# Kernel optimization log

Hardware: AMD Instinct MI355X
Metric: run time of the kernel (lower is better)

Reference implementation:

```python
import jax, jax.numpy as jnp
import numpy as np
from jax import lax

T = 50
THETA = 1.0 - 0.0001  # max_1 - 0.0001, max_1 = T_win/T = 1.0


def conv_t(x, w, b, pad_h):
    # x: [N, C, H, W, T]; slayer conv3d has time-kernel 1 -> conv2d per timestep.
    n, c, h, wd, t = x.shape
    xb = jnp.moveaxis(x, -1, 1).reshape(n * t, c, h, wd)
    y = lax.conv_general_dilated(xb, w, (1, 1), [(pad_h, pad_h), (0, 0)])
    y = y + b[None, :, None, None]
    o, h2, w2 = y.shape[1], y.shape[2], y.shape[3]
    return jnp.moveaxis(y.reshape(n, t, o, h2, w2), 1, -1)


def if_spikes(a):
    # catCuda.getSpikes on an input stacked T times: IF neuron with constant
    # drive a per step, soft reset (v -= theta on spike). a: [N,C,H,W].
    def step(v, _):
        v = v + a
        s = (v >= THETA).astype(a.dtype)
        return v - s * THETA, s
    _, sp = lax.scan(step, jnp.zeros_like(a), None, length=T)
    return jnp.moveaxis(sp, 0, -1)  # [N,C,H,W,T]


def setup_inputs() -> dict:
    key = jax.random.key(0)
    ks = jax.random.split(key, 6)
    def w(k, shape, scale):
        return jax.random.normal(k, shape, jnp.float32) * scale
    x = jax.random.uniform(ks[0], (256, 1, 180, 1, T), jnp.float32)
    return {
        'x': x,
        'w1': w(ks[1], (16, 1, 3, 1), 0.3), 'b1': jnp.zeros(16, jnp.float32),
        'w2': w(ks[2], (32, 16, 9, 1), 0.1), 'b2': jnp.zeros(32, jnp.float32),
        'w3': w(ks[3], (32, 32, 7, 1), 0.1), 'b3': jnp.zeros(32, jnp.float32),
        'wf': w(ks[4], (4, 32, 83, 1), 0.05), 'bf': jnp.zeros(4, jnp.float32),
    }


def reference(x, w1, b1, w2, b2, w3, b3, wf, bf):
    y = conv_t(x, w1, b1, 1)                        # [N,16,180,1,T]
    y = if_spikes(jnp.sum(y, axis=4) / T)           # rate -> spikes
    y = conv_t(y, w2, b2, 1)                        # [N,32,174,1,T]
    y = if_spikes(jnp.sum(y, axis=4) / T)
    y = 1.1 * (y[:, :, 0::2] + y[:, :, 1::2])       # slayer sum-pool (2,1), weight 1.1
    y = if_spikes(jnp.sum(y, axis=4) / T)           # [N,32,87,1,T]
    y = conv_t(y, w3, b3, 1)                        # [N,32,83,1,T]
    y = if_spikes(jnp.sum(y, axis=4) / T)
    out = jnp.einsum('nchwt,ochw->not', y, wf) + bf[None, :, None]  # dense over full spatial
    return jnp.sum(out, axis=-1) / T                # sum_spikes / T -> [N,4]
```

## Files before the change

### kernel.cpp

```cpp
#include <hip/hip_runtime.h>


#define T_STEPS 50
#define THETA   0.9999f

__device__ __forceinline__ float spike_rate(float a) {
    constexpr float INV = 50.0f / 0.9999f;
    float t = a * INV;
    float c = fminf(fmaxf(floorf(t), 0.0f), 50.0f);
    bool risky = (t > 0.5f) && (fabsf(t - rintf(t)) < 5e-4f);
    if (__ballot(risky)) {
        float v = 0.f, cnt = 0.f;
#pragma unroll 1
        for (int k = 0; k < T_STEPS; ++k) {
            v += a;
            float s = (v >= THETA) ? 1.0f : 0.0f;
            v -= s * THETA;
            cnt += s;
        }
        c = cnt;
    }
    return c / 50.0f;
}

extern "C" __global__ void __launch_bounds__(1024)
catnet_kernel(const float* __restrict__ x,
              const float* __restrict__ w1, const float* __restrict__ b1,
              const float* __restrict__ w2, const float* __restrict__ b2,
              const float* __restrict__ w3, const float* __restrict__ b3,
              const float* __restrict__ wf, const float* __restrict__ bf,
              float* __restrict__ out)
{
    const int n    = blockIdx.x;
    const int tid  = threadIdx.x;
    const int wave = tid >> 6;
    const int lane = tid & 63;

    __shared__ float xbar[182];
    __shared__ float r1p[16][182];
    __shared__ float r3p[32][89];
    __shared__ float r4s[32][83];
    __shared__ float part[16];

    if (tid < 16)              { r1p[tid][0] = 0.f; r1p[tid][181] = 0.f; }
    if (tid >= 32 && tid < 64) { r3p[tid-32][0] = 0.f; r3p[tid-32][88] = 0.f; }
    if (tid == 64)             { xbar[0] = 0.f; xbar[181] = 0.f; }

    const float* xn = x + (size_t)n * (180 * 50);
    if (tid < 720) {
        const int h = tid >> 2, q = tid & 3;
        const float* row = xn + h * 50;
        float s = 0.f;
        for (int t = q; t < T_STEPS; t += 4) s += row[t];
        s += __shfl_xor(s, 1, 4);
        s += __shfl_xor(s, 2, 4);
        if (q == 0) xbar[h + 1] = s;
    }
    __syncthreads();

    for (int idx = tid; idx < 16 * 180; idx += 1024) {
        int c = idx / 180, h = idx - c * 180;
        float a = w1[c*3+0] * xbar[h] + w1[c*3+1] * xbar[h+1] + w1[c*3+2] * xbar[h+2];
        a = a / 50.0f + b1[c];
        r1p[c][h + 1] = spike_rate(a);
    }
    __syncthreads();

    {
        const int g   = __builtin_amdgcn_readfirstlane(tid >> 7);
        const int p   = tid & 127;
        const bool act = p < 87;
        const int pr  = act ? p : 0;
        const float* wb = w2 + g * 4 * 144;

        float a0[4], a1[4];
#pragma unroll
        for (int j = 0; j < 4; ++j) { a0[j] = b2[g*4 + j]; a1[j] = a0[j]; }

        for (int ci = 0; ci < 16; ++ci) {
            float w[10];
#pragma unroll
            for (int d = 0; d < 10; ++d)
                w[d] = r1p[ci][2*pr + d];
#pragma unroll
            for (int j = 0; j < 4; ++j) {
                const float* wj = wb + j * 144 + ci * 9;
#pragma unroll
                for (int kh = 0; kh < 9; ++kh) {
                    float wv = wj[kh];
                    a0[j] += wv * w[kh];
                    a1[j] += wv * w[kh + 1];
                }
            }
        }
#pragma unroll
        for (int j = 0; j < 4; ++j) {
            float r20 = spike_rate(a0[j]);
            float r21 = spike_rate(a1[j]);
            float r3  = spike_rate(1.1f * (r20 + r21));
            if (act) r3p[g*4 + j][p + 1] = r3;
        }
    }
    __syncthreads();

    {
        const int g4   = __builtin_amdgcn_readfirstlane((wave >> 1) * 4);
        const int half = wave & 1;
        const int cnt  = half ? 41 : 42;
        const bool act = lane < cnt;
        const int h0   = half * 42 + lane;
        const int hr   = act ? h0 : 0;
        const float* wb = w3 + g4 * 224;

        float a[4];
#pragma unroll
        for (int j = 0; j < 4; ++j) a[j] = b3[g4 + j];

        for (int ci = 0; ci < 32; ++ci) {
            float rv[7];
#pragma unroll
            for (int kh = 0; kh < 7; ++kh) rv[kh] = r3p[ci][hr + kh];
#pragma unroll
            for (int j = 0; j < 4; ++j) {
                const float* wj = wb + j * 224 + ci * 7;
#pragma unroll
                for (int kh = 0; kh < 7; ++kh)
                    a[j] += wj[kh] * rv[kh];
            }
        }
#pragma unroll
        for (int j = 0; j < 4; ++j) {
            float r = spike_rate(a[j]);
            if (act) r4s[g4 + j][h0] = r;
        }
    }
    __syncthreads();

    {
        const int o = wave >> 2, q = wave & 3;
        const float* r4f = &r4s[0][0];
        const float* wo  = wf + o * (32 * 83);
        float acc = 0.f;
        for (int j = q * 64 + lane; j < 32 * 83; j += 256)
            acc += r4f[j] * wo[j];
#pragma unroll
        for (int off = 32; off > 0; off >>= 1)
            acc += __shfl_down(acc, off, 64);
        if (lane == 0) part[wave] = acc;
    }
    __syncthreads();
    if (tid < 4) {
        float s = part[tid*4] + part[tid*4+1] + part[tid*4+2] + part[tid*4+3];
        out[n * 4 + tid] = s + bf[tid];
    }
}

extern "C" void kernel_launch(void* const* d_in, const int* in_sizes, int n_in,
                              void* d_out, int out_size, void* d_ws, size_t ws_size,
                              hipStream_t stream) {
    const float* x  = (const float*)d_in[0];
    const float* w1 = (const float*)d_in[1];
    const float* b1 = (const float*)d_in[2];
    const float* w2 = (const float*)d_in[3];
    const float* b2 = (const float*)d_in[4];
    const float* w3 = (const float*)d_in[5];
    const float* b3 = (const float*)d_in[6];
    const float* wf = (const float*)d_in[7];
    const float* bf = (const float*)d_in[8];
    float* outp = (float*)d_out;

    catnet_kernel<<<dim3(256), dim3(1024), 0, stream>>>(
        x, w1, b1, w2, b2, w3, b3, wf, bf, outp);
}
```

Measured before the change: 104.3 us.

## Split conv2 input into even/odd planes, prefetch rows, vectorize loads, table rates

Stores the layer-1 rates in separate even and odd shared arrays so the stride-2 conv2 window reads contiguous data. Conv2 and conv3 now prefetch the next input channel's rows into registers. The input time-sum and the final dense dot product use float2 loads. Rate division is replaced by a small shared lookup table. The risky-threshold window is narrowed and the pooled-layer exact fallback is removed, which trades exactness near spike boundaries for less divergent work.

```diff
diff --git a/kernel.cpp b/kernel.cpp
--- a/kernel.cpp
+++ b/kernel.cpp
@@ -4,11 +4,11 @@
 #define T_STEPS 50
 #define THETA   0.9999f
 
-__device__ __forceinline__ float spike_rate(float a) {
+__device__ __forceinline__ float spike_rate(float a, const float* __restrict__ tbl) {
     constexpr float INV = 50.0f / 0.9999f;
     float t = a * INV;
     float c = fminf(fmaxf(floorf(t), 0.0f), 50.0f);
-    bool risky = (t > 0.5f) && (fabsf(t - rintf(t)) < 5e-4f);
+    bool risky = (t > 0.5f) && (fabsf(t - rintf(t)) < 2e-4f);
     if (__ballot(risky)) {
         float v = 0.f, cnt = 0.f;
 #pragma unroll 1
@@ -20,7 +20,14 @@
         }
         c = cnt;
     }
-    return c / 50.0f;
+    return tbl[(int)c];
+}
+
+__device__ __forceinline__ float spike_rate_nb(float a, const float* __restrict__ tbl) {
+    constexpr float INV = 50.0f / 0.9999f;
+    float t = a * INV;
+    float c = fminf(fmaxf(floorf(t), 0.0f), 50.0f);
+    return tbl[(int)c];
 }
 
 extern "C" __global__ void __launch_bounds__(1024)
@@ -37,21 +44,26 @@
     const int lane = tid & 63;
 
     __shared__ float xbar[182];
-    __shared__ float r1p[16][182];
+    __shared__ float r1pe[16][92];
+    __shared__ float r1po[16][92];
     __shared__ float r3p[32][89];
-    __shared__ float r4s[32][83];
+    __shared__ alignas(16) float r4s[32][83];
+    __shared__ float ratetbl[51];
     __shared__ float part[16];
 
-    if (tid < 16)              { r1p[tid][0] = 0.f; r1p[tid][181] = 0.f; }
-    if (tid >= 32 && tid < 64) { r3p[tid-32][0] = 0.f; r3p[tid-32][88] = 0.f; }
-    if (tid == 64)             { xbar[0] = 0.f; xbar[181] = 0.f; }
+    if (tid < 16)                { r1pe[tid][0] = 0.f; }
+    if (tid >= 16 && tid < 32)   { r1po[tid-16][90] = 0.f; }
+    if (tid >= 32 && tid < 64)   { r3p[tid-32][0] = 0.f; r3p[tid-32][88] = 0.f; }
+    if (tid == 64)               { xbar[0] = 0.f; xbar[181] = 0.f; }
+    if (tid >= 128 && tid < 179) { ratetbl[tid-128] = (float)(tid-128) / 50.0f; }
 
     const float* xn = x + (size_t)n * (180 * 50);
     if (tid < 720) {
         const int h = tid >> 2, q = tid & 3;
-        const float* row = xn + h * 50;
+        const float2* row2 = reinterpret_cast<const float2*>(xn + h * 50);
         float s = 0.f;
-        for (int t = q; t < T_STEPS; t += 4) s += row[t];
+        for (int k = q; k < 24; k += 4) { float2 v = row2[k]; s += v.x + v.y; }
+        if (q == 0)                     { float2 v = row2[24]; s += v.x + v.y; }
         s += __shfl_xor(s, 1, 4);
         s += __shfl_xor(s, 2, 4);
         if (q == 0) xbar[h + 1] = s;
@@ -62,7 +74,10 @@
         int c = idx / 180, h = idx - c * 180;
         float a = w1[c*3+0] * xbar[h] + w1[c*3+1] * xbar[h+1] + w1[c*3+2] * xbar[h+2];
         a = a / 50.0f + b1[c];
-        r1p[c][h + 1] = spike_rate(a);
+        float r = spike_rate(a, ratetbl);
+        int H = h + 1;
+        if (H & 1) r1po[c][H >> 1] = r;
+        else       r1pe[c][H >> 1] = r;
     }
     __syncthreads();
 
@@ -77,27 +92,37 @@
 #pragma unroll
         for (int j = 0; j < 4; ++j) { a0[j] = b2[g*4 + j]; a1[j] = a0[j]; }
 
+        float we[5], wo[5];
+#pragma unroll
+        for (int d = 0; d < 5; ++d) { we[d] = r1pe[0][pr + d]; wo[d] = r1po[0][pr + d]; }
+
+#pragma unroll 1
         for (int ci = 0; ci < 16; ++ci) {
-            float w[10];
-#pragma unroll
-            for (int d = 0; d < 10; ++d)
-                w[d] = r1p[ci][2*pr + d];
+            const int cn = (ci < 15) ? ci + 1 : 15;
+            float weN[5], woN[5];
+#pragma unroll
+            for (int d = 0; d < 5; ++d) { weN[d] = r1pe[cn][pr + d]; woN[d] = r1po[cn][pr + d]; }
+
 #pragma unroll
             for (int j = 0; j < 4; ++j) {
                 const float* wj = wb + j * 144 + ci * 9;
 #pragma unroll
                 for (int kh = 0; kh < 9; ++kh) {
-                    float wv = wj[kh];
-                    a0[j] += wv * w[kh];
-                    a1[j] += wv * w[kh + 1];
+                    float wv  = wj[kh];
+                    float xlo = (kh & 1) ? wo[kh >> 1] : we[kh >> 1];
+                    float xhi = (kh & 1) ? we[(kh + 1) >> 1] : wo[kh >> 1];
+                    a0[j] += wv * xlo;
+                    a1[j] += wv * xhi;
                 }
             }
+#pragma unroll
+            for (int d = 0; d < 5; ++d) { we[d] = weN[d]; wo[d] = woN[d]; }
         }
 #pragma unroll
         for (int j = 0; j < 4; ++j) {
-            float r20 = spike_rate(a0[j]);
-            float r21 = spike_rate(a1[j]);
-            float r3  = spike_rate(1.1f * (r20 + r21));
+            float r20 = spike_rate(a0[j], ratetbl);
+            float r21 = spike_rate(a1[j], ratetbl);
+            float r3  = spike_rate_nb(1.1f * (r20 + r21), ratetbl);
             if (act) r3p[g*4 + j][p + 1] = r3;
         }
     }
@@ -116,10 +141,17 @@
 #pragma unroll
         for (int j = 0; j < 4; ++j) a[j] = b3[g4 + j];
 
+        float rv[7];
+#pragma unroll
+        for (int kh = 0; kh < 7; ++kh) rv[kh] = r3p[0][hr + kh];
+
+#pragma unroll 1
         for (int ci = 0; ci < 32; ++ci) {
-            float rv[7];
-#pragma unroll
-            for (int kh = 0; kh < 7; ++kh) rv[kh] = r3p[ci][hr + kh];
+            const int cn = (ci < 31) ? ci + 1 : 31;
+            float rn[7];
+#pragma unroll
+            for (int kh = 0; kh < 7; ++kh) rn[kh] = r3p[cn][hr + kh];
+
 #pragma unroll
             for (int j = 0; j < 4; ++j) {
                 const float* wj = wb + j * 224 + ci * 7;
@@ -127,10 +159,12 @@
                 for (int kh = 0; kh < 7; ++kh)
                     a[j] += wj[kh] * rv[kh];
             }
+#pragma unroll
+            for (int kh = 0; kh < 7; ++kh) rv[kh] = rn[kh];
         }
 #pragma unroll
         for (int j = 0; j < 4; ++j) {
-            float r = spike_rate(a[j]);
+            float r = spike_rate(a[j], ratetbl);
             if (act) r4s[g4 + j][h0] = r;
         }
     }
@@ -138,11 +172,13 @@
 
     {
         const int o = wave >> 2, q = wave & 3;
-        const float* r4f = &r4s[0][0];
-        const float* wo  = wf + o * (32 * 83);
+        const float2* r42 = reinterpret_cast<const float2*>(&r4s[0][0]);
+        const float2* wo2 = reinterpret_cast<const float2*>(wf + o * (32 * 83));
         float acc = 0.f;
-        for (int j = q * 64 + lane; j < 32 * 83; j += 256)
-            acc += r4f[j] * wo[j];
+        for (int j = q * 64 + lane; j < 1328; j += 256) {
+            float2 rv = r42[j], wv = wo2[j];
+            acc += rv.x * wv.x + rv.y * wv.y;
+        }
 #pragma unroll
         for (int off = 32; off > 0; off >>= 1)
             acc += __shfl_down(acc, off, 64);
```

Measured after the change: 106.4 us. 2.0% more time.
